# Kernel optimization log

Measured on AMD Instinct MI355X. Metric: run time of the kernel, lower is better.

The kernel has to match this reference:

```python
import jax, jax.numpy as jnp
import numpy as np

B, N, D = 2, 1024, 64
H, DK, DV = 4, 16, 16
DOUT = 128
STEPS = 3


def _ln(x, eps, w=None, b=None):
    mu = jnp.mean(x, axis=-1, keepdims=True)
    var = jnp.mean((x - mu) ** 2, axis=-1, keepdims=True)
    y = (x - mu) * jax.lax.rsqrt(var + eps)
    if w is not None:
        y = y * w + b
    return y


def setup_inputs() -> dict:
    key = jax.random.key(0)
    ks = jax.random.split(key, 16)
    q_x = jax.random.normal(ks[0], (B, N, D), jnp.float32)
    v_x = jax.random.normal(ks[1], (B, N, D), jnp.float32)
    qa = jax.random.uniform(ks[2], (B, N, N), jnp.float32)
    va = jax.random.uniform(ks[3], (B, N, N), jnp.float32)
    q_adj = qa / jnp.sum(qa, axis=-1, keepdims=True)  # row-normalized adjacency
    v_adj = va / jnp.sum(va, axis=-1, keepdims=True)
    s = 0.05
    w_qs = jax.random.normal(ks[4], (D, H * DK), jnp.float32) * s
    w_ks = jax.random.normal(ks[5], (D, H * DK), jnp.float32) * s
    w_vs = jax.random.normal(ks[6], (D, H * DV), jnp.float32) * s
    w_fc = jax.random.normal(ks[7], (H * DV, D), jnp.float32) * s
    mha_ln_w = jnp.ones((D,), jnp.float32)
    mha_ln_b = jnp.zeros((D,), jnp.float32)
    conv_w = jax.random.normal(ks[8], (D, DOUT), jnp.float32) * s
    conv_b = jnp.zeros((DOUT,), jnp.float32)
    lin_w = jax.random.normal(ks[9], (DOUT, D), jnp.float32) * s
    lin_b = jnp.zeros((D,), jnp.float32)
    norm_w = jnp.ones((D,), jnp.float32)
    norm_b = jnp.zeros((D,), jnp.float32)
    return dict(q_x=q_x, q_adj=q_adj, v_x=v_x, v_adj=v_adj,
                w_qs=w_qs, w_ks=w_ks, w_vs=w_vs, w_fc=w_fc,
                mha_ln_w=mha_ln_w, mha_ln_b=mha_ln_b,
                conv_w=conv_w, conv_b=conv_b, lin_w=lin_w, lin_b=lin_b,
                norm_w=norm_w, norm_b=norm_b)


def reference(q_x, q_adj, v_x, v_adj, w_qs, w_ks, w_vs, w_fc,
              mha_ln_w, mha_ln_b, conv_w, conv_b, lin_w, lin_b,
              norm_w, norm_b):
    b, n, d = q_x.shape
    residual = q_x
    qs, vs = [q_x], [v_x]
    q1 = jnp.einsum('bij,bjd->bid', q_adj, q_x)
    v1 = jnp.einsum('bij,bjd->bid', v_adj, v_x)
    qs.append(q1); vs.append(v1)
    for _ in range(2, STEPS):
        q1 = jnp.einsum('bij,bjd->bid', q_adj, q1)
        v1 = jnp.einsum('bij,bjd->bid', v_adj, v1)
        qs.append(q1); vs.append(v1)
    qc = _ln(jnp.concatenate(qs, axis=1), 1e-5)  # [b, STEPS*n, d]
    vc = _ln(jnp.concatenate(vs, axis=1), 1e-5)
    L = qc.shape[1]
    # multi-head attention (dropout = identity in eval)
    q = (qc @ w_qs).reshape(b, L, H, DK)
    k = (qc @ w_ks).reshape(b, L, H, DK)
    v = (vc @ w_vs).reshape(b, L, H, DV)
    scores = jnp.einsum('bqhd,bkhd->bhqk', q, k) / jnp.asarray(DK ** 0.5, q.dtype)
    attn = jax.nn.softmax(scores, axis=-1)
    o = jnp.einsum('bhqk,bkhd->bqhd', attn, v).reshape(b, L, H * DV)
    o = o @ w_fc + qc
    o = _ln(o, 1e-6, mha_ln_w, mha_ln_b)
    # pool across diffusion steps (faithful to original reshape semantics)
    x = jnp.mean(o.reshape(b, n, -1, STEPS), axis=-1)  # [b, n, d]
    x1 = jax.nn.relu(x @ conv_w + conv_b)
    x = residual + x1 @ lin_w + lin_b
    return _ln(x, 1e-5, norm_w, norm_b)
```

## Files before the change

kernel.cpp:

```cpp
#include <hip/hip_runtime.h>
#include <hip/hip_bf16.h>

#define B_ 2
#define N_ 1024
#define D_ 64
#define L_ 3072
#define H_ 4

typedef __attribute__((ext_vector_type(8))) short s8v;
typedef __attribute__((ext_vector_type(4))) short s4v;
typedef __attribute__((ext_vector_type(4))) float f32x4;

#define EXP2F(x) __builtin_amdgcn_exp2f(x)
#define QSCALE 0.36067376022224085f

__device__ __forceinline__ float wave_sum64(float v) {
#pragma unroll
    for (int off = 32; off > 0; off >>= 1) v += __shfl_xor(v, off, 64);
    return v;
}

__device__ __forceinline__ short f2bf(float f) {
    unsigned u = __float_as_uint(f);
    u += 0x7FFFu + ((u >> 16) & 1u);
    return (short)(u >> 16);
}

__device__ __forceinline__ s8v ldfrag_pad(const __hip_bfloat16* p) {
    s4v lo4 = *reinterpret_cast<const s4v*>(p);
    s8v r;
    r[0] = lo4[0]; r[1] = lo4[1]; r[2] = lo4[2]; r[3] = lo4[3];
    r[4] = 0; r[5] = 0; r[6] = 0; r[7] = 0;
    return r;
}
__device__ __forceinline__ s8v ldfrag_full(const __hip_bfloat16* p0, const __hip_bfloat16* p1) {
    s4v a = *reinterpret_cast<const s4v*>(p0);
    s4v b = *reinterpret_cast<const s4v*>(p1);
    s8v r;
    r[0] = a[0]; r[1] = a[1]; r[2] = a[2]; r[3] = a[3];
    r[4] = b[0]; r[5] = b[1]; r[6] = b[2]; r[7] = b[3];
    return r;
}
__device__ __forceinline__ s8v wfrag_build(const float* __restrict__ W, int N, int ct, int ks,
                                           int lo, int hi, float scale) {
    s8v r;
    int n = ct * 16 + lo;
    int k0 = ks * 32 + 4 * hi;
#pragma unroll
    for (int j = 0; j < 4; ++j) {
        r[j]     = f2bf(W[(k0 + j) * N + n] * scale);
        r[4 + j] = f2bf(W[(k0 + 16 + j) * N + n] * scale);
    }
    return r;
}

__global__ void spmm16(const float* __restrict__ adj_q, const float* __restrict__ src_q,
                       float* __restrict__ dst_q,
                       const float* __restrict__ adj_v, const float* __restrict__ src_v,
                       float* __restrict__ dst_v) {
    const int tid = threadIdx.x;
    const int ty = tid >> 4;
    const int tx = tid & 15;
    const int i0 = blockIdx.x * 16;
    const int qv = blockIdx.y;
    const int b  = blockIdx.z;
    const float* adj = qv ? adj_v : adj_q;
    const float* src = qv ? src_v : src_q;
    float*       dst = qv ? dst_v : dst_q;
    adj += (size_t)b * N_ * N_;
    src += (size_t)b * N_ * D_;
    dst += (size_t)b * N_ * D_;

    __shared__ float xs[64][64];
    __shared__ float as[16][68];

    float acc0 = 0.f, acc1 = 0.f, acc2 = 0.f, acc3 = 0.f;
    for (int k0 = 0; k0 < N_; k0 += 64) {
#pragma unroll
        for (int i = 0; i < 4; ++i) {
            int f = tid + i * 256;
            int r = f >> 4, c4 = f & 15;
            float4 v = *reinterpret_cast<const float4*>(src + (size_t)(k0 + r) * D_ + c4 * 4);
            *reinterpret_cast<float4*>(&xs[r][c4 * 4]) = v;
        }
        {
            int r = tid >> 4, c4 = tid & 15;
            float4 v = *reinterpret_cast<const float4*>(adj + (size_t)(i0 + r) * N_ + k0 + c4 * 4);
            *reinterpret_cast<float4*>(&as[r][c4 * 4]) = v;
        }
        __syncthreads();
#pragma unroll
        for (int jj = 0; jj < 64; ++jj) {
            float4 xv = *reinterpret_cast<const float4*>(&xs[jj][tx * 4]);
            float a = as[ty][jj];
            acc0 += a * xv.x; acc1 += a * xv.y; acc2 += a * xv.z; acc3 += a * xv.w;
        }
        __syncthreads();
    }
    float4 o; o.x = acc0; o.y = acc1; o.z = acc2; o.w = acc3;
    *reinterpret_cast<float4*>(dst + (size_t)(i0 + ty) * D_ + tx * 4) = o;
}

__global__ void concat_ln(const float* __restrict__ qx, const float* __restrict__ q1,
                          const float* __restrict__ q2,
                          const float* __restrict__ vx, const float* __restrict__ v1,
                          const float* __restrict__ v2,
                          float* __restrict__ qc,
                          __hip_bfloat16* __restrict__ qcb, __hip_bfloat16* __restrict__ vcb) {
    int rid  = blockIdx.x * 4 + (threadIdx.x >> 6);
    int lane = threadIdx.x & 63;
    int qvsel = rid >= (B_ * L_);
    int r = qvsel ? rid - B_ * L_ : rid;
    int b = r / L_, l = r % L_;
    int s = l / N_, i = l % N_;
    const float* src;
    if (!qvsel) src = (s == 0) ? qx : (s == 1) ? q1 : q2;
    else        src = (s == 0) ? vx : (s == 1) ? v1 : v2;
    float v = src[((size_t)b * N_ + i) * D_ + lane];
    float mean = wave_sum64(v) * (1.0f / 64.0f);
    float d = v - mean;
    float var = wave_sum64(d * d) * (1.0f / 64.0f);
    float y = d * rsqrtf(var + 1e-5f);
    size_t o = ((size_t)b * L_ + l) * D_ + lane;
    if (!qvsel) {
        qc[o] = y;
        reinterpret_cast<short*>(qcb)[o] = f2bf(y);
    } else {
        reinterpret_cast<short*>(vcb)[o] = f2bf(y);
    }
}

__global__ __launch_bounds__(256) void gemm_qkv(
        const __hip_bfloat16* __restrict__ qcb, const __hip_bfloat16* __restrict__ vcb,
        const float* __restrict__ wq, const float* __restrict__ wk, const float* __restrict__ wv,
        __hip_bfloat16* __restrict__ qb, __hip_bfloat16* __restrict__ kb,
        __hip_bfloat16* __restrict__ vtb) {
    const int w = threadIdx.x >> 6;
    const int lane = threadIdx.x & 63;
    const int lo = lane & 15, hi = lane >> 4;
    const int ct0 = w * 3;

    s8v wf[3][2];
#pragma unroll
    for (int c = 0; c < 3; ++c) {
        int ct = ct0 + c;
        const float* W = (ct < 4) ? wq : (ct < 8) ? wk : wv;
        float sc = (ct < 4) ? QSCALE : 1.0f;
        wf[c][0] = wfrag_build(W, 64, ct & 3, 0, lo, hi, sc);
        wf[c][1] = wfrag_build(W, 64, ct & 3, 1, lo, hi, sc);
    }
    const bool needq = (ct0 < 8);
    const bool needv = (ct0 + 2 >= 8);
    const f32x4 zz = {0.f, 0.f, 0.f, 0.f};

#pragma unroll
    for (int rr = 0; rr < 2; ++rr) {
        int rt = blockIdx.x * 2 + rr;
        int rbase = rt * 16;
        int b = rbase / L_;
        int l = rbase % L_ + lo;
        s8v aq0, aq1, av0, av1;
        if (needq) {
            const __hip_bfloat16* ar = qcb + (size_t)(rbase + lo) * 64;
            aq0 = ldfrag_full(ar + 4 * hi, ar + 16 + 4 * hi);
            aq1 = ldfrag_full(ar + 32 + 4 * hi, ar + 48 + 4 * hi);
        }
        if (needv) {
            const __hip_bfloat16* ar = vcb + (size_t)(rbase + lo) * 64;
            av0 = ldfrag_full(ar + 4 * hi, ar + 16 + 4 * hi);
            av1 = ldfrag_full(ar + 32 + 4 * hi, ar + 48 + 4 * hi);
        }
#pragma unroll
        for (int c = 0; c < 3; ++c) {
            int ct = ct0 + c;
            f32x4 acc = zz;
            if (ct < 8) {
                acc = __builtin_amdgcn_mfma_f32_16x16x32_bf16(wf[c][0], aq0, acc, 0, 0, 0);
                acc = __builtin_amdgcn_mfma_f32_16x16x32_bf16(wf[c][1], aq1, acc, 0, 0, 0);
                __hip_bfloat16* dst = (ct < 4) ? qb : kb;
                int h = ct & 3;
                s4v o;
                o[0] = f2bf(acc[0]); o[1] = f2bf(acc[1]); o[2] = f2bf(acc[2]); o[3] = f2bf(acc[3]);
                *reinterpret_cast<s4v*>(reinterpret_cast<short*>(dst) +
                    ((size_t)(b * H_ + h) * L_ + l) * 16 + 4 * hi) = o;
            } else {
                acc = __builtin_amdgcn_mfma_f32_16x16x32_bf16(wf[c][0], av0, acc, 0, 0, 0);
                acc = __builtin_amdgcn_mfma_f32_16x16x32_bf16(wf[c][1], av1, acc, 0, 0, 0);
                int h = ct - 8;
                short* vt = reinterpret_cast<short*>(vtb);
#pragma unroll
                for (int j = 0; j < 4; ++j) {
                    int dv = 4 * hi + j;
                    vt[((size_t)(b * H_ + h) * 16 + dv) * L_ + l] = f2bf(acc[j]);
                }
            }
        }
    }
}

__global__ __launch_bounds__(256) void attn_mfma(
        const __hip_bfloat16* __restrict__ qb, const __hip_bfloat16* __restrict__ kb,
        const __hip_bfloat16* __restrict__ vtb, __hip_bfloat16* __restrict__ attnob) {
    const int lane = threadIdx.x & 63;
    const int w = threadIdx.x >> 6;
    const int g = blockIdx.x;
    const int bh = g / 96;
    const int tp = g % 96;
    const int b = bh >> 2, h = bh & 3;
    const int lo = lane & 15, hi = lane >> 4;
    const int q0 = tp * 32;

    const __hip_bfloat16* qbase = qb + (size_t)bh * L_ * 16;
    const __hip_bfloat16* kbase = kb + (size_t)bh * L_ * 16;
    const __hip_bfloat16* vtbase = vtb + ((size_t)bh * 16 + lo) * L_;

    s8v qfA = ldfrag_pad(qbase + (size_t)(q0 + lo) * 16 + 4 * hi);
    s8v qfB = ldfrag_pad(qbase + (size_t)(q0 + 16 + lo) * 16 + 4 * hi);

    f32x4 accA = {0.f, 0.f, 0.f, 0.f}, accB = {0.f, 0.f, 0.f, 0.f};
    float lsA = 0.f, lsB = 0.f;
    const f32x4 zz = {0.f, 0.f, 0.f, 0.f};

    const int kbeg = w * (L_ / 4), kend = kbeg + (L_ / 4);
    for (int kt = kbeg; kt < kend; kt += 32) {
        s8v kf0 = ldfrag_pad(kbase + (size_t)(kt + lo) * 16 + 4 * hi);
        s8v kf1 = ldfrag_pad(kbase + (size_t)(kt + 16 + lo) * 16 + 4 * hi);
        s8v vf  = ldfrag_full(vtbase + kt + 4 * hi, vtbase + kt + 16 + 4 * hi);

        f32x4 s0A = __builtin_amdgcn_mfma_f32_16x16x32_bf16(kf0, qfA, zz, 0, 0, 0);
        f32x4 s1A = __builtin_amdgcn_mfma_f32_16x16x32_bf16(kf1, qfA, zz, 0, 0, 0);
        f32x4 s0B = __builtin_amdgcn_mfma_f32_16x16x32_bf16(kf0, qfB, zz, 0, 0, 0);
        f32x4 s1B = __builtin_amdgcn_mfma_f32_16x16x32_bf16(kf1, qfB, zz, 0, 0, 0);

        float pA0 = EXP2F(s0A[0]), pA1 = EXP2F(s0A[1]), pA2 = EXP2F(s0A[2]), pA3 = EXP2F(s0A[3]);
        float pA4 = EXP2F(s1A[0]), pA5 = EXP2F(s1A[1]), pA6 = EXP2F(s1A[2]), pA7 = EXP2F(s1A[3]);
        float pB0 = EXP2F(s0B[0]), pB1 = EXP2F(s0B[1]), pB2 = EXP2F(s0B[2]), pB3 = EXP2F(s0B[3]);
        float pB4 = EXP2F(s1B[0]), pB5 = EXP2F(s1B[1]), pB6 = EXP2F(s1B[2]), pB7 = EXP2F(s1B[3]);
        lsA += ((pA0 + pA1) + (pA2 + pA3)) + ((pA4 + pA5) + (pA6 + pA7));
        lsB += ((pB0 + pB1) + (pB2 + pB3)) + ((pB4 + pB5) + (pB6 + pB7));

        s8v pfA, pfB;
        pfA[0] = f2bf(pA0); pfA[1] = f2bf(pA1); pfA[2] = f2bf(pA2); pfA[3] = f2bf(pA3);
        pfA[4] = f2bf(pA4); pfA[5] = f2bf(pA5); pfA[6] = f2bf(pA6); pfA[7] = f2bf(pA7);
        pfB[0] = f2bf(pB0); pfB[1] = f2bf(pB1); pfB[2] = f2bf(pB2); pfB[3] = f2bf(pB3);
        pfB[4] = f2bf(pB4); pfB[5] = f2bf(pB5); pfB[6] = f2bf(pB6); pfB[7] = f2bf(pB7);

        accA = __builtin_amdgcn_mfma_f32_16x16x32_bf16(vf, pfA, accA, 0, 0, 0);
        accB = __builtin_amdgcn_mfma_f32_16x16x32_bf16(vf, pfB, accB, 0, 0, 0);
    }

    lsA += __shfl_xor(lsA, 16, 64); lsA += __shfl_xor(lsA, 32, 64);
    lsB += __shfl_xor(lsB, 16, 64); lsB += __shfl_xor(lsB, 32, 64);

    __shared__ float red[4][2][64][5];
    red[w][0][lane][0] = accA[0]; red[w][0][lane][1] = accA[1];
    red[w][0][lane][2] = accA[2]; red[w][0][lane][3] = accA[3];
    red[w][0][lane][4] = lsA;
    red[w][1][lane][0] = accB[0]; red[w][1][lane][1] = accB[1];
    red[w][1][lane][2] = accB[2]; red[w][1][lane][3] = accB[3];
    red[w][1][lane][4] = lsB;
    __syncthreads();
    if (w < 2) {
        int t = w;
        float a0 = 0.f, a1 = 0.f, a2 = 0.f, a3 = 0.f, lt = 0.f;
#pragma unroll
        for (int ww = 0; ww < 4; ++ww) {
            a0 += red[ww][t][lane][0];
            a1 += red[ww][t][lane][1];
            a2 += red[ww][t][lane][2];
            a3 += red[ww][t][lane][3];
            lt += red[ww][t][lane][4];
        }
        float inv = 1.0f / lt;
        s4v o;
        o[0] = f2bf(a0 * inv); o[1] = f2bf(a1 * inv); o[2] = f2bf(a2 * inv); o[3] = f2bf(a3 * inv);
        *reinterpret_cast<s4v*>(reinterpret_cast<short*>(attnob) +
            ((size_t)b * L_ + q0 + t * 16 + lo) * 64 + h * 16 + 4 * hi) = o;
    }
}

__global__ __launch_bounds__(256) void gemm_fc_ln(
        const __hip_bfloat16* __restrict__ attnob, const float* __restrict__ qc,
        const float* __restrict__ wfc,
        const float* __restrict__ lnw, const float* __restrict__ lnb,
        float* __restrict__ o2) {
    const int rt = blockIdx.x * 4 + (threadIdx.x >> 6);
    const int lane = threadIdx.x & 63;
    const int lo = lane & 15, hi = lane >> 4;
    const f32x4 zz = {0.f, 0.f, 0.f, 0.f};

    s8v wf[4][2];
#pragma unroll
    for (int ct = 0; ct < 4; ++ct) {
        wf[ct][0] = wfrag_build(wfc, 64, ct, 0, lo, hi, 1.0f);
        wf[ct][1] = wfrag_build(wfc, 64, ct, 1, lo, hi, 1.0f);
    }
    const __hip_bfloat16* ar = attnob + (size_t)(rt * 16 + lo) * 64;
    s8v a0 = ldfrag_full(ar + 4 * hi, ar + 16 + 4 * hi);
    s8v a1 = ldfrag_full(ar + 32 + 4 * hi, ar + 48 + 4 * hi);

    f32x4 acc[4];
    const int row = rt * 16 + lo;
#pragma unroll
    for (int ct = 0; ct < 4; ++ct) {
        acc[ct] = zz;
        acc[ct] = __builtin_amdgcn_mfma_f32_16x16x32_bf16(wf[ct][0], a0, acc[ct], 0, 0, 0);
        acc[ct] = __builtin_amdgcn_mfma_f32_16x16x32_bf16(wf[ct][1], a1, acc[ct], 0, 0, 0);
        f32x4 rq = *reinterpret_cast<const f32x4*>(qc + (size_t)row * 64 + ct * 16 + 4 * hi);
        acc[ct][0] += rq[0]; acc[ct][1] += rq[1]; acc[ct][2] += rq[2]; acc[ct][3] += rq[3];
    }
    float s = 0.f;
#pragma unroll
    for (int ct = 0; ct < 4; ++ct) s += (acc[ct][0] + acc[ct][1]) + (acc[ct][2] + acc[ct][3]);
    s += __shfl_xor(s, 16, 64); s += __shfl_xor(s, 32, 64);
    float mean = s * (1.0f / 64.0f);
    float vs = 0.f;
#pragma unroll
    for (int ct = 0; ct < 4; ++ct) {
#pragma unroll
        for (int j = 0; j < 4; ++j) { float d = acc[ct][j] - mean; vs += d * d; }
    }
    vs += __shfl_xor(vs, 16, 64); vs += __shfl_xor(vs, 32, 64);
    float rsq = rsqrtf(vs * (1.0f / 64.0f) + 1e-6f);
#pragma unroll
    for (int ct = 0; ct < 4; ++ct) {
        f32x4 w4 = *reinterpret_cast<const f32x4*>(lnw + ct * 16 + 4 * hi);
        f32x4 b4 = *reinterpret_cast<const f32x4*>(lnb + ct * 16 + 4 * hi);
        f32x4 o;
#pragma unroll
        for (int j = 0; j < 4; ++j) o[j] = (acc[ct][j] - mean) * rsq * w4[j] + b4[j];
        *reinterpret_cast<f32x4*>(o2 + (size_t)row * 64 + ct * 16 + 4 * hi) = o;
    }
}

__global__ void pool_k(const float* __restrict__ o2, __hip_bfloat16* __restrict__ xb) {
    int rid  = blockIdx.x * 4 + (threadIdx.x >> 6);
    int lane = threadIdx.x & 63;
    int b = rid / N_, i = rid % N_;
    const float* ob = o2 + (size_t)b * L_ * 64 + (size_t)192 * i;
    int t = 3 * lane;
    float xv = (ob[t] + ob[t + 1] + ob[t + 2]) * (1.0f / 3.0f);
    reinterpret_cast<short*>(xb)[(size_t)rid * 64 + lane] = f2bf(xv);
}

__global__ __launch_bounds__(256) void gemm_conv(
        const __hip_bfloat16* __restrict__ xb, const float* __restrict__ convw,
        const float* __restrict__ convb, __hip_bfloat16* __restrict__ x1b) {
    const int w = threadIdx.x >> 6;
    const int lane = threadIdx.x & 63;
    const int lo = lane & 15, hi = lane >> 4;
    const int rt = blockIdx.x;
    const f32x4 zz = {0.f, 0.f, 0.f, 0.f};

    s8v wf[2][2];
#pragma unroll
    for (int c = 0; c < 2; ++c) {
        int ct = 2 * w + c;
        wf[c][0] = wfrag_build(convw, 128, ct, 0, lo, hi, 1.0f);
        wf[c][1] = wfrag_build(convw, 128, ct, 1, lo, hi, 1.0f);
    }
    const __hip_bfloat16* ar = xb + (size_t)(rt * 16 + lo) * 64;
    s8v a0 = ldfrag_full(ar + 4 * hi, ar + 16 + 4 * hi);
    s8v a1 = ldfrag_full(ar + 32 + 4 * hi, ar + 48 + 4 * hi);

#pragma unroll
    for (int c = 0; c < 2; ++c) {
        int ct = 2 * w + c;
        f32x4 acc = zz;
        acc = __builtin_amdgcn_mfma_f32_16x16x32_bf16(wf[c][0], a0, acc, 0, 0, 0);
        acc = __builtin_amdgcn_mfma_f32_16x16x32_bf16(wf[c][1], a1, acc, 0, 0, 0);
        f32x4 bia = *reinterpret_cast<const f32x4*>(convb + ct * 16 + 4 * hi);
        s4v o;
#pragma unroll
        for (int j = 0; j < 4; ++j) o[j] = f2bf(fmaxf(acc[j] + bia[j], 0.f));
        *reinterpret_cast<s4v*>(reinterpret_cast<short*>(x1b) +
            (size_t)(rt * 16 + lo) * 128 + ct * 16 + 4 * hi) = o;
    }
}

__global__ __launch_bounds__(256) void gemm_lin_ln(
        const __hip_bfloat16* __restrict__ x1b, const float* __restrict__ qx,
        const float* __restrict__ linw, const float* __restrict__ linb,
        const float* __restrict__ nw, const float* __restrict__ nb,
        float* __restrict__ out) {
    const int rt = blockIdx.x * 4 + (threadIdx.x >> 6);
    const int lane = threadIdx.x & 63;
    const int lo = lane & 15, hi = lane >> 4;
    const f32x4 zz = {0.f, 0.f, 0.f, 0.f};

    s8v wf[4][4];
#pragma unroll
    for (int ct = 0; ct < 4; ++ct)
#pragma unroll
        for (int ks = 0; ks < 4; ++ks)
            wf[ct][ks] = wfrag_build(linw, 64, ct, ks, lo, hi, 1.0f);

    const __hip_bfloat16* ar = x1b + (size_t)(rt * 16 + lo) * 128;
    s8v af[4];
#pragma unroll
    for (int ks = 0; ks < 4; ++ks)
        af[ks] = ldfrag_full(ar + ks * 32 + 4 * hi, ar + ks * 32 + 16 + 4 * hi);

    f32x4 acc[4];
    const int row = rt * 16 + lo;
#pragma unroll
    for (int ct = 0; ct < 4; ++ct) {
        acc[ct] = zz;
#pragma unroll
        for (int ks = 0; ks < 4; ++ks)
            acc[ct] = __builtin_amdgcn_mfma_f32_16x16x32_bf16(wf[ct][ks], af[ks], acc[ct], 0, 0, 0);
        f32x4 bia = *reinterpret_cast<const f32x4*>(linb + ct * 16 + 4 * hi);
        f32x4 rq  = *reinterpret_cast<const f32x4*>(qx + (size_t)row * 64 + ct * 16 + 4 * hi);
#pragma unroll
        for (int j = 0; j < 4; ++j) acc[ct][j] += bia[j] + rq[j];
    }
    float s = 0.f;
#pragma unroll
    for (int ct = 0; ct < 4; ++ct) s += (acc[ct][0] + acc[ct][1]) + (acc[ct][2] + acc[ct][3]);
    s += __shfl_xor(s, 16, 64); s += __shfl_xor(s, 32, 64);
    float mean = s * (1.0f / 64.0f);
    float vs = 0.f;
#pragma unroll
    for (int ct = 0; ct < 4; ++ct) {
#pragma unroll
        for (int j = 0; j < 4; ++j) { float d = acc[ct][j] - mean; vs += d * d; }
    }
    vs += __shfl_xor(vs, 16, 64); vs += __shfl_xor(vs, 32, 64);
    float rsq = rsqrtf(vs * (1.0f / 64.0f) + 1e-5f);
#pragma unroll
    for (int ct = 0; ct < 4; ++ct) {
        f32x4 w4 = *reinterpret_cast<const f32x4*>(nw + ct * 16 + 4 * hi);
        f32x4 b4 = *reinterpret_cast<const f32x4*>(nb + ct * 16 + 4 * hi);
        f32x4 o;
#pragma unroll
        for (int j = 0; j < 4; ++j) o[j] = (acc[ct][j] - mean) * rsq * w4[j] + b4[j];
        *reinterpret_cast<f32x4*>(out + (size_t)row * 64 + ct * 16 + 4 * hi) = o;
    }
}

extern "C" void kernel_launch(void* const* d_in, const int* in_sizes, int n_in,
                              void* d_out, int out_size, void* d_ws, size_t ws_size,
                              hipStream_t stream) {
    const float* q_x      = (const float*)d_in[0];
    const float* q_adj    = (const float*)d_in[1];
    const float* v_x      = (const float*)d_in[2];
    const float* v_adj    = (const float*)d_in[3];
    const float* w_qs     = (const float*)d_in[4];
    const float* w_ks     = (const float*)d_in[5];
    const float* w_vs     = (const float*)d_in[6];
    const float* w_fc     = (const float*)d_in[7];
    const float* mha_ln_w = (const float*)d_in[8];
    const float* mha_ln_b = (const float*)d_in[9];
    const float* conv_w   = (const float*)d_in[10];
    const float* conv_b   = (const float*)d_in[11];
    const float* lin_w    = (const float*)d_in[12];
    const float* lin_b    = (const float*)d_in[13];
    const float* norm_w   = (const float*)d_in[14];
    const float* norm_b   = (const float*)d_in[15];

    float* ws = (float*)d_ws;
    float* q1    = ws;
    float* v1    = q1 + 131072;
    float* q2    = v1 + 131072;
    float* v2    = q2 + 131072;
    float* qc    = v2 + 131072;
    __hip_bfloat16* qcb    = (__hip_bfloat16*)(qc + 393216);
    __hip_bfloat16* vcb    = qcb + 393216;
    __hip_bfloat16* qb     = vcb + 393216;
    __hip_bfloat16* kb     = qb + 393216;
    __hip_bfloat16* vtb    = kb + 393216;
    __hip_bfloat16* attnob = vtb + 393216;
    float* o2    = (float*)(attnob + 393216);
    __hip_bfloat16* xb     = (__hip_bfloat16*)(o2 + 393216);
    __hip_bfloat16* x1b    = xb + 131072;
    float* out   = (float*)d_out;

    spmm16<<<dim3(64, 2, 2), 256, 0, stream>>>(q_adj, q_x, q1, v_adj, v_x, v1);
    spmm16<<<dim3(64, 2, 2), 256, 0, stream>>>(q_adj, q1, q2, v_adj, v1, v2);
    concat_ln<<<3072, 256, 0, stream>>>(q_x, q1, q2, v_x, v1, v2, qc, qcb, vcb);
    gemm_qkv<<<192, 256, 0, stream>>>(qcb, vcb, w_qs, w_ks, w_vs, qb, kb, vtb);
    attn_mfma<<<768, 256, 0, stream>>>(qb, kb, vtb, attnob);
    gemm_fc_ln<<<96, 256, 0, stream>>>(attnob, qc, w_fc, mha_ln_w, mha_ln_b, o2);
    pool_k<<<512, 256, 0, stream>>>(o2, xb);
    gemm_conv<<<128, 256, 0, stream>>>(xb, conv_w, conv_b, x1b);
    gemm_lin_ln<<<32, 256, 0, stream>>>(x1b, q_x, lin_w, lin_b, norm_w, norm_b, out);
}
```

Baseline: 180.4 us.

## Replace FP32 adjacency SpMM with bf16 MFMA using pre-transposed features

Swaps the shared-memory FP32 adjacency-times-features kernel for an MFMA bf16 kernel. A new transpose kernel converts the input features to bf16 in a feature-major layout, and the first diffusion step also writes its output transposed in bf16 to feed the second step. Adjacency rows are read straight from global memory and converted to bf16 in registers. This moves the dense N×N products onto matrix cores, at the cost of bf16 precision in the diffusion and an extra launch for the transpose.

```diff
diff --git a/kernel.cpp b/kernel.cpp
--- a/kernel.cpp
+++ b/kernel.cpp
@@ -54,51 +54,71 @@
     return r;
 }
 
-__global__ void spmm16(const float* __restrict__ adj_q, const float* __restrict__ src_q,
-                       float* __restrict__ dst_q,
-                       const float* __restrict__ adj_v, const float* __restrict__ src_v,
-                       float* __restrict__ dst_v) {
-    const int tid = threadIdx.x;
-    const int ty = tid >> 4;
-    const int tx = tid & 15;
-    const int i0 = blockIdx.x * 16;
-    const int qv = blockIdx.y;
-    const int b  = blockIdx.z;
-    const float* adj = qv ? adj_v : adj_q;
-    const float* src = qv ? src_v : src_q;
-    float*       dst = qv ? dst_v : dst_q;
-    adj += (size_t)b * N_ * N_;
-    src += (size_t)b * N_ * D_;
-    dst += (size_t)b * N_ * D_;
-
-    __shared__ float xs[64][64];
-    __shared__ float as[16][68];
-
-    float acc0 = 0.f, acc1 = 0.f, acc2 = 0.f, acc3 = 0.f;
-    for (int k0 = 0; k0 < N_; k0 += 64) {
-#pragma unroll
-        for (int i = 0; i < 4; ++i) {
-            int f = tid + i * 256;
-            int r = f >> 4, c4 = f & 15;
-            float4 v = *reinterpret_cast<const float4*>(src + (size_t)(k0 + r) * D_ + c4 * 4);
-            *reinterpret_cast<float4*>(&xs[r][c4 * 4]) = v;
-        }
-        {
-            int r = tid >> 4, c4 = tid & 15;
-            float4 v = *reinterpret_cast<const float4*>(adj + (size_t)(i0 + r) * N_ + k0 + c4 * 4);
-            *reinterpret_cast<float4*>(&as[r][c4 * 4]) = v;
-        }
-        __syncthreads();
-#pragma unroll
-        for (int jj = 0; jj < 64; ++jj) {
-            float4 xv = *reinterpret_cast<const float4*>(&xs[jj][tx * 4]);
-            float a = as[ty][jj];
-            acc0 += a * xv.x; acc1 += a * xv.y; acc2 += a * xv.z; acc3 += a * xv.w;
-        }
-        __syncthreads();
-    }
-    float4 o; o.x = acc0; o.y = acc1; o.z = acc2; o.w = acc3;
-    *reinterpret_cast<float4*>(dst + (size_t)(i0 + ty) * D_ + tx * 4) = o;
+__global__ void xpose(const float* __restrict__ xq, const float* __restrict__ xv,
+                      __hip_bfloat16* __restrict__ xtq, __hip_bfloat16* __restrict__ xtv) {
+    __shared__ short ts[64][65];
+    int m = blockIdx.y;
+    int qv = m >> 1, b = m & 1;
+    int l0 = blockIdx.x * 64;
+    const float* x = (qv ? xv : xq) + (size_t)b * N_ * 64;
+    int t = threadIdx.x;
+#pragma unroll
+    for (int i = 0; i < 4; ++i) {
+        int f = t + i * 256;
+        int r = f >> 4, c4 = f & 15;
+        float4 v = *reinterpret_cast<const float4*>(x + (size_t)(l0 + r) * 64 + c4 * 4);
+        ts[c4 * 4 + 0][r] = f2bf(v.x);
+        ts[c4 * 4 + 1][r] = f2bf(v.y);
+        ts[c4 * 4 + 2][r] = f2bf(v.z);
+        ts[c4 * 4 + 3][r] = f2bf(v.w);
+    }
+    __syncthreads();
+    short* xt = reinterpret_cast<short*>(qv ? xtv : xtq) + (size_t)b * 64 * N_;
+#pragma unroll
+    for (int i = 0; i < 4; ++i) {
+        int f = t + i * 256;
+        int d = f >> 4, seg = f & 15;
+        s4v o;
+        o[0] = ts[d][seg * 4 + 0]; o[1] = ts[d][seg * 4 + 1];
+        o[2] = ts[d][seg * 4 + 2]; o[3] = ts[d][seg * 4 + 3];
+        *reinterpret_cast<s4v*>(xt + (size_t)d * N_ + l0 + seg * 4) = o;
+    }
+}
+
+__global__ __launch_bounds__(256) void spmm_mfma(
+        const float* __restrict__ adj_q, const float* __restrict__ adj_v,
+        const __hip_bfloat16* __restrict__ xtq, const __hip_bfloat16* __restrict__ xtv,
+        float* __restrict__ oq, float* __restrict__ ov,
+        __hip_bfloat16* __restrict__ oqt, __hip_bfloat16* __restrict__ ovt, int writet) {
+    const int lane = threadIdx.x & 63;
+    const int w = threadIdx.x >> 6;
+    const int lo = lane & 15, hi = lane >> 4;
+    const int rt = blockIdx.x;
+    const int qv = blockIdx.y, b = blockIdx.z;
+
+    const float* adj = (qv ? adj_v : adj_q) + (size_t)b * N_ * N_ + (size_t)(rt * 16 + lo) * N_;
+    const __hip_bfloat16* xt = (qv ? xtv : xtq) + ((size_t)b * 64 + w * 16 + lo) * N_;
+
+    f32x4 acc = {0.f, 0.f, 0.f, 0.f};
+#pragma unroll 8
+    for (int ks = 0; ks < 32; ++ks) {
+        int k0 = ks * 32;
+        float4 a4 = *reinterpret_cast<const float4*>(adj + k0 + 4 * hi);
+        float4 b4 = *reinterpret_cast<const float4*>(adj + k0 + 16 + 4 * hi);
+        s8v af;
+        af[0] = f2bf(a4.x); af[1] = f2bf(a4.y); af[2] = f2bf(a4.z); af[3] = f2bf(a4.w);
+        af[4] = f2bf(b4.x); af[5] = f2bf(b4.y); af[6] = f2bf(b4.z); af[7] = f2bf(b4.w);
+        s8v xf = ldfrag_full(xt + k0 + 4 * hi, xt + k0 + 16 + 4 * hi);
+        acc = __builtin_amdgcn_mfma_f32_16x16x32_bf16(xf, af, acc, 0, 0, 0);
+    }
+    float* o = (qv ? ov : oq) + ((size_t)b * N_ + rt * 16 + lo) * 64 + w * 16 + 4 * hi;
+    *reinterpret_cast<f32x4*>(o) = acc;
+    if (writet) {
+        short* ot = reinterpret_cast<short*>(qv ? ovt : oqt) + (size_t)b * 64 * N_;
+#pragma unroll
+        for (int j = 0; j < 4; ++j)
+            ot[(size_t)(w * 16 + 4 * hi + j) * N_ + rt * 16 + lo] = f2bf(acc[j]);
+    }
 }
 
 __global__ void concat_ln(const float* __restrict__ qx, const float* __restrict__ q1,
@@ -464,19 +484,26 @@
     float* q2    = v1 + 131072;
     float* v2    = q2 + 131072;
     float* qc    = v2 + 131072;
-    __hip_bfloat16* qcb    = (__hip_bfloat16*)(qc + 393216);
+    float* o2    = qc + 393216;
+    __hip_bfloat16* qcb    = (__hip_bfloat16*)(o2 + 393216);
     __hip_bfloat16* vcb    = qcb + 393216;
     __hip_bfloat16* qb     = vcb + 393216;
     __hip_bfloat16* kb     = qb + 393216;
     __hip_bfloat16* vtb    = kb + 393216;
     __hip_bfloat16* attnob = vtb + 393216;
-    float* o2    = (float*)(attnob + 393216);
-    __hip_bfloat16* xb     = (__hip_bfloat16*)(o2 + 393216);
+    __hip_bfloat16* xtq    = attnob + 393216;
+    __hip_bfloat16* xtv    = xtq + 131072;
+    __hip_bfloat16* q1t    = xtv + 131072;
+    __hip_bfloat16* v1t    = q1t + 131072;
+    __hip_bfloat16* xb     = v1t + 131072;
     __hip_bfloat16* x1b    = xb + 131072;
     float* out   = (float*)d_out;
 
-    spmm16<<<dim3(64, 2, 2), 256, 0, stream>>>(q_adj, q_x, q1, v_adj, v_x, v1);
-    spmm16<<<dim3(64, 2, 2), 256, 0, stream>>>(q_adj, q1, q2, v_adj, v1, v2);
+    xpose<<<dim3(16, 4), 256, 0, stream>>>(q_x, v_x, xtq, xtv);
+    spmm_mfma<<<dim3(64, 2, 2), 256, 0, stream>>>(q_adj, v_adj, xtq, xtv,
+                                                  q1, v1, q1t, v1t, 1);
+    spmm_mfma<<<dim3(64, 2, 2), 256, 0, stream>>>(q_adj, v_adj, q1t, v1t,
+                                                  q2, v2, nullptr, nullptr, 0);
     concat_ln<<<3072, 256, 0, stream>>>(q_x, q1, q2, v_x, v1, v2, qc, qcb, vcb);
     gemm_qkv<<<192, 256, 0, stream>>>(qcb, vcb, w_qs, w_ks, w_vs, qb, kb, vtb);
     attn_mfma<<<768, 256, 0, stream>>>(qb, kb, vtb, attnob);
```

After: 177.0 us. About the same (-1.9%).
